# Kernel optimization log

Hardware: AMD Instinct MI355X
Metric: run time of the kernel (lower is better)

The kernel has to match this reference:

```python
import jax, jax.numpy as jnp
import numpy as np

B, N, S, K = 16, 4096, 1024, 32
C_PTS = 64
MLP = [64, 64, 128]
EPS = 1e-5


def setup_inputs() -> dict:
    key = jax.random.key(0)
    ks = jax.random.split(key, 2 + len(MLP))
    inp = {
        "xyz": jax.random.normal(ks[0], (B, N, 3), jnp.float32),
        "points": jax.random.normal(ks[1], (B, N, C_PTS), jnp.float32),
    }
    last = 3 + C_PTS
    for i, o in enumerate(MLP):
        inp[f"w{i}"] = jax.random.normal(ks[2 + i], (o, last), jnp.float32) / np.sqrt(last).astype(np.float32)
        inp[f"b{i}"] = jnp.zeros((o,), jnp.float32)
        inp[f"gamma{i}"] = jnp.ones((o,), jnp.float32)
        inp[f"beta{i}"] = jnp.zeros((o,), jnp.float32)
        last = o
    return inp


def _farthest_point_sample(xyz, n_samples):
    # Sequential FPS; start index 0 (torch version uses a random start).
    b, n, _ = xyz.shape

    def step(carry, _):
        distance, farthest = carry  # [B,N], [B]
        centroid = jnp.take_along_axis(xyz, farthest[:, None, None], axis=1)  # [B,1,3]
        dist = jnp.sum((xyz - centroid) ** 2, axis=-1)  # [B,N]
        distance = jnp.minimum(distance, dist)
        new_far = jnp.argmax(distance, axis=-1).astype(jnp.int32)
        return (distance, new_far), farthest

    init = (jnp.full((b, n), 1e10, xyz.dtype), jnp.zeros((b,), jnp.int32))
    _, idxs = jax.lax.scan(step, init, None, length=n_samples)
    return idxs.T  # [B,S]


def _square_distance(src, dst):
    # ||src||^2 + ||dst||^2 - 2 src.dst  -> [B, S, N]
    return (jnp.sum(src ** 2, -1)[:, :, None]
            + jnp.sum(dst ** 2, -1)[:, None, :]
            - 2.0 * jnp.einsum('bsc,bnc->bsn', src, dst))


_gather = jax.vmap(lambda a, i: a[i])  # per-batch fancy gather


def _mlp_layer(x, w, bias, gamma, beta):
    # x: [B,S,K,Cin]; 1x1 conv == channel matmul, then training-mode BN over (B,S,K), then ReLU.
    y = jnp.einsum('bskc,oc->bsko', x, w) + bias
    mean = jnp.mean(y, axis=(0, 1, 2))
    var = jnp.mean((y - mean) ** 2, axis=(0, 1, 2))
    y = (y - mean) * jax.lax.rsqrt(var + EPS) * gamma + beta
    return jax.nn.relu(y)


def reference(xyz, points, w0, b0, gamma0, beta0, w1, b1, gamma1, beta1, w2, b2, gamma2, beta2):
    fps_idx = _farthest_point_sample(xyz, S)                   # [B,S]
    new_xyz = _gather(xyz, fps_idx)                            # [B,S,3]
    dists = _square_distance(new_xyz, xyz)                     # [B,S,N]
    nn_idx = jax.lax.top_k(-dists, K)[1]                       # [B,S,K]
    grouped_xyz = _gather(xyz, nn_idx)                         # [B,S,K,3]
    grouped_pts = _gather(points, nn_idx)                      # [B,S,K,C]
    feat = jnp.concatenate([grouped_xyz - new_xyz[:, :, None, :], grouped_pts], axis=-1)  # [B,S,K,3+C]
    x = _mlp_layer(feat, w0, b0, gamma0, beta0)
    x = _mlp_layer(x, w1, b1, gamma1, beta1)
    x = _mlp_layer(x, w2, b2, gamma2, beta2)
    new_points = jnp.max(x, axis=2)                            # [B,S,Cout]
    new_points = jnp.transpose(new_points, (0, 2, 1))          # [B,Cout,S] matches torch output
    return new_xyz, new_points
```

## Files before the change

kernel.cpp:

```cpp
#include <hip/hip_runtime.h>

#define B_ 16
#define N_ 4096
#define S_ 1024
#define K_ 32
#define NSLOT 128
#define CNT_F 524288.0f
#define RWS 524288

typedef unsigned short ushort_t;
typedef short short8 __attribute__((ext_vector_type(8)));
typedef float floatx4 __attribute__((ext_vector_type(4)));
union U4S8 { uint4 u; short8 v; };

__device__ __forceinline__ ushort_t f2bf(float f) {
  unsigned u = __float_as_uint(f);
  unsigned r = (u + 0x7fffu + ((u >> 16) & 1u)) >> 16;
  return (ushort_t)r;
}
__device__ __forceinline__ unsigned pkrne(float a, float b) {
  return (unsigned)f2bf(a) | ((unsigned)f2bf(b) << 16);
}
__device__ __forceinline__ unsigned pkhu(float a, float b) {
  return ((__float_as_uint(a) + 0x8000u) >> 16) |
// ... 14 lines not shown
  x1 = fmaxf(fmaf(x1, sca.y, sha.y), 0.0f);
  x2 = fmaxf(fmaf(x2, sca.z, sha.z), 0.0f);
  x3 = fmaxf(fmaf(x3, sca.w, sha.w), 0.0f);
  x4 = fmaxf(fmaf(x4, scb.x, shb.x), 0.0f);
  x5 = fmaxf(fmaf(x5, scb.y, shb.y), 0.0f);
  x6 = fmaxf(fmaf(x6, scb.z, shb.z), 0.0f);
  x7 = fmaxf(fmaf(x7, scb.w, shb.w), 0.0f);
  return make_uint4(pkhu(x0, x1), pkhu(x2, x3), pkhu(x4, x5), pkhu(x6, x7));
}

#define FPS_T 256
#define FPS_P (N_ / FPS_T)
#define FPS_W (FPS_T / 64)

template <int CTRL>
__device__ __forceinline__ unsigned dpp_max_u32(unsigned v) {
  unsigned o = (unsigned)__builtin_amdgcn_update_dpp(0, (int)v, CTRL, 0xf, 0xf, true);
  return v > o ? v : o;
}
__device__ __forceinline__ unsigned wave_max_u32(unsigned v) {
  v = dpp_max_u32<0x111>(v);
  v = dpp_max_u32<0x112>(v);
  v = dpp_max_u32<0x114>(v);
  v = dpp_max_u32<0x118>(v);
  v = dpp_max_u32<0x142>(v);
  v = dpp_max_u32<0x143>(v);
  return (unsigned)__builtin_amdgcn_readlane((int)v, 63);
}

__global__ __launch_bounds__(256) void prep_all(
    const float* __restrict__ xyz, float4* __restrict__ xyzw,
    const float* __restrict__ w0, const float* __restrict__ w1,
    const float* __restrict__ w2, ushort_t* __restrict__ wB0,
    ushort_t* __restrict__ wB1, ushort_t* __restrict__ wB2) {
  int i = blockIdx.x * 256 + threadIdx.x;
  float x = xyz[(size_t)i * 3 + 0];
  float y = xyz[(size_t)i * 3 + 1];
  float z = xyz[(size_t)i * 3 + 2];
  float nrm = __fadd_rn(__fadd_rn(__fmul_rn(x, x), __fmul_rn(y, y)), __fmul_rn(z, z));
  xyzw[i] = make_float4(x, y, z, nrm);
  if (i < 64 * 96) {
    int o = i / 96, c = i % 96;
    ushort_t v = 0;
    if (c < 64) v = f2bf(w0[o * 67 + 3 + c]);
    else if (c < 67) v = f2bf(w0[o * 67 + (c - 64)]);
    wB0[i] = v;
  }
  if (i < 64 * 64) wB1[i] = f2bf(w1[i]);
  if (i < 128 * 64) wB2[i] = f2bf(w2[i]);
}

#define SMEM_BYTES 56320
#define NBLK 512
#define NCONS_W ((NBLK - B_) * 4)

__global__ __launch_bounds__(256, 1) void fused_kernel(
    const float* __restrict__ xyz, const float* __restrict__ points,
    const float4* __restrict__ xyzw, const ushort_t* __restrict__ wB0,
    const float* __restrict__ bias0, int* __restrict__ pub,
    float* __restrict__ out_newxyz, ushort_t* __restrict__ y0,
    float* __restrict__ stats) {
  __shared__ __align__(16) char smem[SMEM_BYTES];
  int t = threadIdx.x;
  int w = t >> 6, l = t & 63;

  if (blockIdx.x < B_) {
    float* xyz_s = (float*)smem;
    int* idx_s = (int*)(smem + 49152);
    unsigned long long* keys_s = (unsigned long long*)(smem + 53248);
    int b = blockIdx.x;
    const float* xb = xyz + (size_t)b * N_ * 3;
    for (int i = t; i < N_ * 3; i += FPS_T) xyz_s[i] = xb[i];
    __syncthreads();
    float px[FPS_P], py[FPS_P], pz[FPS_P], dd[FPS_P];
#pragma unroll
    for (int j = 0; j < FPS_P; ++j) {
      int n = t + j * FPS_T;
      px[j] = xyz_s[n * 3 + 0];
      py[j] = xyz_s[n * 3 + 1];
      pz[j] = xyz_s[n * 3 + 2];
      dd[j] = 1e10f;
    }
    __builtin_amdgcn_s_setprio(3);
    int fi = 0;
#pragma unroll 1
    for (int s = 0; s < S_; ++s) {
      if (t == 0) {
        idx_s[s] = fi;
        __hip_atomic_store(&pub[(b << 10) + s], fi + 1, __ATOMIC_RELAXED,
                           __HIP_MEMORY_SCOPE_AGENT);
      }
      float cx = xyz_s[fi * 3 + 0], cy = xyz_s[fi * 3 + 1], cz = xyz_s[fi * 3 + 2];
      float bv = -1.0f;
      int bi = 0;
#pragma unroll
      for (int j = 0; j < FPS_P; ++j) {
        float dx = __fsub_rn(px[j], cx);
        float dy = __fsub_rn(py[j], cy);
        float dz = __fsub_rn(pz[j], cz);
        float d = __fadd_rn(__fadd_rn(__fmul_rn(dx, dx), __fmul_rn(dy, dy)),
                            __fmul_rn(dz, dz));
        d = fminf(dd[j], d);
        dd[j] = d;
        if (d > bv) { bv = d; bi = t + j * FPS_T; }
      }
      unsigned hi = __float_as_uint(bv);
      unsigned vmax = wave_max_u32(hi);
      unsigned cand = (hi == vmax) ? (unsigned)(N_ - 1 - bi) : 0u;
      unsigned cmax = wave_max_u32(cand);
      if ((t & 63) == 0)
        keys_s[(s & 1) * FPS_W + (t >> 6)] =
            ((unsigned long long)vmax << 32) | cmax;
      __syncthreads();
      unsigned long long m = keys_s[(s & 1) * FPS_W + 0];
#pragma unroll
      for (int ww = 1; ww < FPS_W; ++ww) {
        unsigned long long k = keys_s[(s & 1) * FPS_W + ww];
        m = k > m ? k : m;
      }
      fi = (N_ - 1) - (int)(unsigned)(m & 0xFFFFFFFFULL);
    }
    __builtin_amdgcn_s_setprio(0);
    __syncthreads();
    for (int s = t; s < S_; s += FPS_T) {
      int i = idx_s[s];
      out_newxyz[((size_t)b * S_ + s) * 3 + 0] = xyz_s[i * 3 + 0];
      out_newxyz[((size_t)b * S_ + s) * 3 + 1] = xyz_s[i * 3 + 1];
      out_newxyz[((size_t)b * S_ + s) * 3 + 2] = xyz_s[i * 3 + 2];
    }
    return;
  }

  int n16 = l & 15, quad = l >> 4;
  U4S8 bf0[4][3];
  float b0v[4], ssum[4], ssq[4];
#pragma unroll
  for (int nt = 0; nt < 4; ++nt) {
#pragma unroll
    for (int kc = 0; kc < 3; ++kc)
      bf0[nt][kc].u = *reinterpret_cast<const uint4*>(
          wB0 + (size_t)(nt * 16 + n16) * 96 + kc * 32 + quad * 8);
    b0v[nt] = bias0[nt * 16 + n16];
    ssum[nt] = 0.0f;
    ssq[nt] = 0.0f;
  }
  float* ltw = (float*)(smem + w * (16 * 68 * 4));
  int wid = (blockIdx.x - B_) * 4 + w;

#pragma unroll 1
  for (int r = wid; r < B_ * S_; r += NCONS_W) {
    int b = r & 15, s = r >> 4;
    int bs = (b << 10) + s;
    int pv = 0;
    if (l == 0) {
      int tries = 0;
      while ((pv = __hip_atomic_load(&pub[bs], __ATOMIC_RELAXED,
                                     __HIP_MEMORY_SCOPE_AGENT)) == 0) {
        __builtin_amdgcn_s_sleep(32);
        if (++tries > 65536) break;
      }
    }
    pv = __shfl(pv, 0);
    int ci = pv - 1;
    if (ci < 0) ci = 0;
    const float4* xw = xyzw + (size_t)b * N_;
    float4 c4 = xw[ci];
    float sx = c4.x, sy = c4.y, sz = c4.z;
    float nxn = c4.w;

    unsigned u[64];
#pragma unroll
    for (int j = 0; j < 64; ++j) {
      int nn = j * 64 + l;
      float4 v = xw[nn];
      float e = __fadd_rn(__fadd_rn(__fmul_rn(sx, v.x), __fmul_rn(sy, v.y)),
                          __fmul_rn(sz, v.z));
      float d = __fadd_rn(__fadd_rn(nxn, v.w), __fmul_rn(-2.0f, e));
      int sb = __float_as_int(d);
      u[j] = (sb < 0) ? ~((unsigned)sb) : (((unsigned)sb) | 0x80000000u);
    }
// ... 76 lines not shown
#pragma unroll
        for (int rI = 0; rI < 4; ++rI) {
          float ys = acc[nt][rI] + b0v[nt];
          ssum[nt] += ys;
          ssq[nt] = fmaf(ys, ys, ssq[nt]);
          ltw[(quad * 4 + rI) * 68 + nt * 16 + n16] = ys;
        }
      const float* lrow = ltw + n16 * 68 + quad * 16;
      float4 va = *reinterpret_cast<const float4*>(lrow);
      float4 vb = *reinterpret_cast<const float4*>(lrow + 4);
      float4 vc = *reinterpret_cast<const float4*>(lrow + 8);
      float4 vd = *reinterpret_cast<const float4*>(lrow + 12);
      ushort_t* yo = y0 + (size_t)(rb + n16) * 64 + quad * 16;
      *reinterpret_cast<uint4*>(yo) =
          make_uint4(pkhu(va.x, va.y), pkhu(va.z, va.w), pkhu(vb.x, vb.y), pkhu(vb.z, vb.w));
      *reinterpret_cast<uint4*>(yo + 8) =
          make_uint4(pkhu(vc.x, vc.y), pkhu(vc.z, vc.w), pkhu(vd.x, vd.y), pkhu(vd.z, vd.w));
    }
  }

  float* stp = stats + (size_t)(wid & (NSLOT - 1)) * 64 * 2;
#pragma unroll
  for (int nt = 0; nt < 4; ++nt) {
    float s = ssum[nt], q = ssq[nt];
    s += __shfl_down(s, 16); q += __shfl_down(q, 16);
    s += __shfl_down(s, 32); q += __shfl_down(q, 32);
    if (l < 16) {
      atomicAdd(&stp[(size_t)(nt * 16 + l) * 2 + 0], s);
      atomicAdd(&stp[(size_t)(nt * 16 + l) * 2 + 1], q);
    }
  }
}

__global__ __launch_bounds__(256) void gemm1_mfma(
    const ushort_t* __restrict__ y0, const float* __restrict__ bnp,
    const ushort_t* __restrict__ wB1, const float* __restrict__ bias1,
    ushort_t* __restrict__ y1, float* __restrict__ stats) {
  __shared__ __align__(16) float lt[4][16 * 68];
  int t = threadIdx.x;
  int w = t >> 6, l = t & 63;
  int n = l & 15, quad = l >> 4;
  U4S8 bf[4][2];
#pragma unroll
  for (int nt = 0; nt < 4; ++nt)
#pragma unroll
    for (int kc = 0; kc < 2; ++kc)
      bf[nt][kc].u = *reinterpret_cast<const uint4*>(
          wB1 + (size_t)(nt * 16 + n) * 64 + kc * 32 + quad * 8);
  float4 scA[2], scB[2], shA[2], shB[2];
#pragma unroll
  for (int kc = 0; kc < 2; ++kc) {
    int cb = kc * 32 + quad * 8;
    scA[kc] = *reinterpret_cast<const float4*>(&bnp[cb]);
    scB[kc] = *reinterpret_cast<const float4*>(&bnp[cb + 4]);
    shA[kc] = *reinterpret_cast<const float4*>(&bnp[64 + cb]);
    shB[kc] = *reinterpret_cast<const float4*>(&bnp[64 + cb + 4]);
  }
  float b1v[4], ssum[4], ssq[4];
#pragma unroll
  for (int nt = 0; nt < 4; ++nt) {
    b1v[nt] = bias1[nt * 16 + n];
    ssum[nt] = 0.0f;
    ssq[nt] = 0.0f;
  }
  int rowbase0 = blockIdx.x * 1024 + w * 256;
  float* ltw = lt[w];
#pragma unroll 1
  for (int tile = 0; tile < 16; ++tile) {
    int rb = rowbase0 + tile * 16;
    U4S8 af[2];
#pragma unroll
    for (int kc = 0; kc < 2; ++kc) {
      uint4 xv = *reinterpret_cast<const uint4*>(
          y0 + (size_t)(rb + n) * 64 + kc * 32 + quad * 8);
      af[kc].u = bn_relu_pack(xv, scA[kc], scB[kc], shA[kc], shB[kc]);
    }
    floatx4 acc[4];
#pragma unroll
    for (int nt = 0; nt < 4; ++nt) acc[nt] = floatx4{0.f, 0.f, 0.f, 0.f};
#pragma unroll
    for (int kc = 0; kc < 2; ++kc)
#pragma unroll
      for (int nt = 0; nt < 4; ++nt)
        acc[nt] = __builtin_amdgcn_mfma_f32_16x16x32_bf16(
            af[kc].v, bf[nt][kc].v, acc[nt], 0, 0, 0);
#pragma unroll
    for (int nt = 0; nt < 4; ++nt)
#pragma unroll
      for (int rI = 0; rI < 4; ++rI) {
        float ys = acc[nt][rI] + b1v[nt];
        ssum[nt] += ys;
        ssq[nt] = fmaf(ys, ys, ssq[nt]);
        ltw[(quad * 4 + rI) * 68 + nt * 16 + n] = ys;
      }
    const float* lrow = ltw + n * 68 + quad * 16;
    float4 va = *reinterpret_cast<const float4*>(lrow);
    float4 vb = *reinterpret_cast<const float4*>(lrow + 4);
    float4 vc = *reinterpret_cast<const float4*>(lrow + 8);
    float4 vd = *reinterpret_cast<const float4*>(lrow + 12);
    ushort_t* yo = y1 + (size_t)(rb + n) * 64 + quad * 16;
    *reinterpret_cast<uint4*>(yo) =
        make_uint4(pkhu(va.x, va.y), pkhu(va.z, va.w), pkhu(vb.x, vb.y), pkhu(vb.z, vb.w));
    *reinterpret_cast<uint4*>(yo + 8) =
        make_uint4(pkhu(vc.x, vc.y), pkhu(vc.z, vc.w), pkhu(vd.x, vd.y), pkhu(vd.z, vd.w));
  }
  float* stp = stats + (size_t)((blockIdx.x * 4 + w) & (NSLOT - 1)) * 64 * 2;
#pragma unroll
  for (int nt = 0; nt < 4; ++nt) {
    float s = ssum[nt], q = ssq[nt];
    s += __shfl_down(s, 16); q += __shfl_down(q, 16);
    s += __shfl_down(s, 32); q += __shfl_down(q, 32);
    if (l < 16) {
      atomicAdd(&stp[(size_t)(nt * 16 + l) * 2 + 0], s);
      atomicAdd(&stp[(size_t)(nt * 16 + l) * 2 + 1], q);
    }
  }
}

__global__ __launch_bounds__(256) void gemm2_mfma(
    const ushort_t* __restrict__ y1, const float* __restrict__ bnp,
    const ushort_t* __restrict__ wB2, const float* __restrict__ bias2,
    float* __restrict__ stats, float* __restrict__ maxY, float* __restrict__ minY) {
  int t = threadIdx.x;
  int w = t >> 6, l = t & 63;
  int n = l & 15, quad = l >> 4;
  U4S8 bf[8][2];
#pragma unroll
  for (int nt = 0; nt < 8; ++nt)
#pragma unroll
    for (int kc = 0; kc < 2; ++kc)
      bf[nt][kc].u = *reinterpret_cast<const uint4*>(
          wB2 + (size_t)(nt * 16 + n) * 64 + kc * 32 + quad * 8);
  float4 scA[2], scB[2], shA[2], shB[2];
#pragma unroll
  for (int kc = 0; kc < 2; ++kc) {
    int cb = kc * 32 + quad * 8;
    scA[kc] = *reinterpret_cast<const float4*>(&bnp[128 + cb]);
    scB[kc] = *reinterpret_cast<const float4*>(&bnp[128 + cb + 4]);
    shA[kc] = *reinterpret_cast<const float4*>(&bnp[192 + cb]);
    shB[kc] = *reinterpret_cast<const float4*>(&bnp[192 + cb + 4]);
  }
  float b2v[8], ssum[8], ssq[8], mxv[8], mnv[8];
#pragma unroll
  for (int nt = 0; nt < 8; ++nt) {
    b2v[nt] = bias2[nt * 16 + n];
    ssum[nt] = 0.0f;
    ssq[nt] = 0.0f;
    mxv[nt] = -3.4e38f;
    mnv[nt] = 3.4e38f;
  }
  int rowbase0 = blockIdx.x * 1024 + w * 256;
#pragma unroll 1
  for (int tile = 0; tile < 16; ++tile) {
    int rb = rowbase0 + tile * 16;
    U4S8 af[2];
#pragma unroll
    for (int kc = 0; kc < 2; ++kc) {
      uint4 xv = *reinterpret_cast<const uint4*>(
          y1 + (size_t)(rb + n) * 64 + kc * 32 + quad * 8);
      af[kc].u = bn_relu_pack(xv, scA[kc], scB[kc], shA[kc], shB[kc]);
    }
    floatx4 acc[8];
#pragma unroll
    for (int nt = 0; nt < 8; ++nt) acc[nt] = floatx4{0.f, 0.f, 0.f, 0.f};
#pragma unroll
    for (int kc = 0; kc < 2; ++kc)
#pragma unroll
      for (int nt = 0; nt < 8; ++nt)
        acc[nt] = __builtin_amdgcn_mfma_f32_16x16x32_bf16(
            af[kc].v, bf[nt][kc].v, acc[nt], 0, 0, 0);
#pragma unroll
    for (int nt = 0; nt < 8; ++nt)
#pragma unroll
      for (int rI = 0; rI < 4; ++rI) {
        float ya = acc[nt][rI] + b2v[nt];
        ssum[nt] += ya;
        ssq[nt] = fmaf(ya, ya, ssq[nt]);
        mxv[nt] = fmaxf(mxv[nt], ya);
        mnv[nt] = fminf(mnv[nt], ya);
      }
    if (tile & 1) {
      int sidx = (rowbase0 >> 5) + (tile >> 1);
#pragma unroll
      for (int nt = 0; nt < 8; ++nt) {
        float mx = mxv[nt], mn = mnv[nt];
        mx = fmaxf(mx, __shfl_down(mx, 16));
        mn = fminf(mn, __shfl_down(mn, 16));
        mx = fmaxf(mx, __shfl_down(mx, 32));
        mn = fminf(mn, __shfl_down(mn, 32));
        if (l < 16) {
          maxY[(size_t)sidx * 128 + nt * 16 + l] = mx;
          minY[(size_t)sidx * 128 + nt * 16 + l] = mn;
        }
        mxv[nt] = -3.4e38f;
        mnv[nt] = 3.4e38f;
      }
    }
  }
  float* stp = stats + (size_t)((blockIdx.x * 4 + w) & (NSLOT - 1)) * 128 * 2;
#pragma unroll
  for (int nt = 0; nt < 8; ++nt) {
    float s = ssum[nt], q = ssq[nt];
    s += __shfl_down(s, 16); q += __shfl_down(q, 16);
    s += __shfl_down(s, 32); q += __shfl_down(q, 32);
    if (l < 16) {
      atomicAdd(&stp[(size_t)(nt * 16 + l) * 2 + 0], s);
      atomicAdd(&stp[(size_t)(nt * 16 + l) * 2 + 1], q);
    }
  }
}

__global__ void bn_finalize(const float* __restrict__ st, int cout,
                            const float* __restrict__ gamma,
                            const float* __restrict__ beta,
                            float* __restrict__ scale, float* __restrict__ shift) {
  int o = threadIdx.x;
  if (o >= cout) return;
  float s = 0.0f, q = 0.0f;
  for (int i = 0; i < NSLOT; ++i) {
    s += st[((size_t)i * cout + o) * 2 + 0];
    q += st[((size_t)i * cout + o) * 2 + 1];
  }
  float mean = s * (1.0f / CNT_F);
  float var = q * (1.0f / CNT_F) - mean * mean;
  float sc = gamma[o] / sqrtf(var + 1e-5f);
  scale[o] = sc;
  shift[o] = beta[o] - mean * sc;
}

__global__ __launch_bounds__(256) void pool_kernel(
    const float* __restrict__ maxY, const float* __restrict__ minY,
    const float* __restrict__ bnp, float* __restrict__ out) {
  __shared__ float tile[128 * 65];
  int b = blockIdx.x >> 4;
  int sbase = (blockIdx.x & 15) * 64;
  int t = threadIdx.x;
#pragma unroll 4
  for (int i = 0; i < 32; ++i) {
    int e = i * 256 + t;
    int sl = e >> 7, o = e & 127;
    float sc = bnp[256 + o], sh = bnp[384 + o];
    size_t g = ((size_t)(b * S_ + sbase + sl)) * 128 + o;
    float v = (sc >= 0.0f) ? maxY[g] : minY[g];
    tile[o * 65 + sl] = fmaxf(fmaf(v, sc, sh), 0.0f);
  }
  __syncthreads();
  int sl = t & 63;
  for (int o2 = t >> 6; o2 < 128; o2 += 4) {
    out[((size_t)(b * 128 + o2)) * S_ + sbase + sl] = tile[o2 * 65 + sl];
  }
}

static inline size_t alup(size_t x) { return (x + 255) & ~(size_t)255; }

extern "C" void kernel_launch(void* const* d_in, const int* in_sizes, int n_in,
                              void* d_out, int out_size, void* d_ws, size_t ws_size,
                              hipStream_t stream) {
  (void)in_sizes; (void)n_in; (void)out_size;
  const float* xyz = (const float*)d_in[0];
  const float* points = (const float*)d_in[1];
  const float* w0 = (const float*)d_in[2];
  const float* b0 = (const float*)d_in[3];
  const float* g0 = (const float*)d_in[4];
  const float* be0 = (const float*)d_in[5];
  const float* w1 = (const float*)d_in[6];
  const float* b1 = (const float*)d_in[7];
  const float* g1 = (const float*)d_in[8];
  const float* be1 = (const float*)d_in[9];
  const float* w2 = (const float*)d_in[10];
  const float* b2 = (const float*)d_in[11];
  const float* g2 = (const float*)d_in[12];
  const float* be2 = (const float*)d_in[13];
  float* out_newxyz = (float*)d_out;
  float* out_newpts = out_newxyz + (size_t)B_ * S_ * 3;

  char* p = (char*)d_ws;
  int* pub = (int*)p;      p += alup((size_t)B_ * S_ * 4);
  float4* xyzw = (float4*)p; p += alup((size_t)B_ * N_ * 16);
  float* st0 = (float*)p;  p += (size_t)NSLOT * 64 * 2 * 4;
  float* st1 = (float*)p;  p += (size_t)NSLOT * 64 * 2 * 4;
  float* st2 = (float*)p;  p += (size_t)NSLOT * 128 * 2 * 4;
  float* bnp = (float*)p;  p += alup(512 * 4);
  ushort_t* wB0 = (ushort_t*)p; p += alup(64 * 96 * 2);
  ushort_t* wB1 = (ushort_t*)p; p += alup(64 * 64 * 2);
  ushort_t* wB2 = (ushort_t*)p; p += alup(128 * 64 * 2);
  float* maxY = (float*)p; p += (size_t)B_ * S_ * 128 * 4;
  float* minY = (float*)p; p += (size_t)B_ * S_ * 128 * 4;
  ushort_t* y0 = (ushort_t*)p; p += (size_t)RWS * 64 * 2;
  ushort_t* y1 = (ushort_t*)p; p += (size_t)RWS * 64 * 2;
  if ((size_t)(p - (char*)d_ws) > ws_size) return;

  float* sc0 = bnp;       float* sh0 = bnp + 64;
  float* sc1 = bnp + 128; float* sh1 = bnp + 192;
  float* sc2 = bnp + 256; float* sh2 = bnp + 384;

  hipMemsetAsync(st0, 0, (size_t)NSLOT * (64 + 64 + 128) * 2 * 4, stream);
  hipMemsetAsync(pub, 0, (size_t)B_ * S_ * 4, stream);
  prep_all<<<256, 256, 0, stream>>>(xyz, xyzw, w0, w1, w2, wB0, wB1, wB2);
  fused_kernel<<<NBLK, 256, 0, stream>>>(
      xyz, points, xyzw, wB0, b0, pub, out_newxyz, y0, st0);
  bn_finalize<<<1, 128, 0, stream>>>(st0, 64, g0, be0, sc0, sh0);
  gemm1_mfma<<<RWS / 1024, 256, 0, stream>>>(y0, bnp, wB1, b1, y1, st1);
  bn_finalize<<<1, 128, 0, stream>>>(st1, 64, g1, be1, sc1, sh1);
  gemm2_mfma<<<RWS / 1024, 256, 0, stream>>>(y1, bnp, wB2, b2, st2, maxY, minY);
  bn_finalize<<<1, 128, 0, stream>>>(st2, 128, g2, be2, sc2, sh2);
  pool_kernel<<<B_ * (S_ / 64), 256, 0, stream>>>(maxY, minY, bnp, out_newpts);
}
```

Measured before the change: 784.7 us.

## Tree-reduce FPS argmax per thread and idle consumer blocks colocated with FPS blocks

After: 850.3 us. 1.08x slower.

```diff
diff --git a/kernel.cpp b/kernel.cpp
--- a/kernel.cpp
+++ b/kernel.cpp
@@ -90,7 +90,7 @@
 
 #define SMEM_BYTES 56320
 #define NBLK 512
-#define NCONS_W ((NBLK - B_) * 4)
+#define NCONS_W 1920
 
 __global__ __launch_bounds__(256, 1) void fused_kernel(
     const float* __restrict__ xyz, const float* __restrict__ points,
@@ -129,8 +129,6 @@
                            __HIP_MEMORY_SCOPE_AGENT);
       }
       float cx = xyz_s[fi * 3 + 0], cy = xyz_s[fi * 3 + 1], cz = xyz_s[fi * 3 + 2];
-      float bv = -1.0f;
-      int bi = 0;
 #pragma unroll
       for (int j = 0; j < FPS_P; ++j) {
         float dx = __fsub_rn(px[j], cx);
@@ -138,13 +136,27 @@
         float dz = __fsub_rn(pz[j], cz);
         float d = __fadd_rn(__fadd_rn(__fmul_rn(dx, dx), __fmul_rn(dy, dy)),
                             __fmul_rn(dz, dz));
-        d = fminf(dd[j], d);
-        dd[j] = d;
-        if (d > bv) { bv = d; bi = t + j * FPS_T; }
-      }
-      unsigned hi = __float_as_uint(bv);
+        dd[j] = fminf(dd[j], d);
+      }
+      float tm[FPS_P / 2];
+#pragma unroll
+      for (int i = 0; i < FPS_P / 2; ++i) tm[i] = fmaxf(dd[i], dd[i + FPS_P / 2]);
+#pragma unroll
+      for (int st = FPS_P / 4; st >= 1; st >>= 1)
+#pragma unroll
+        for (int i = 0; i < st; ++i) tm[i] = fmaxf(tm[i], tm[i + st]);
+      float lmax = tm[0];
+      unsigned cu[FPS_P];
+#pragma unroll
+      for (int j = 0; j < FPS_P; ++j)
+        cu[j] = (dd[j] == lmax) ? (unsigned)(N_ - 1 - (t + j * FPS_T)) : 0u;
+#pragma unroll
+      for (int st = FPS_P / 2; st >= 1; st >>= 1)
+#pragma unroll
+        for (int i = 0; i < st; ++i) cu[i] = cu[i] > cu[i + st] ? cu[i] : cu[i + st];
+      unsigned hi = __float_as_uint(lmax);
       unsigned vmax = wave_max_u32(hi);
-      unsigned cand = (hi == vmax) ? (unsigned)(N_ - 1 - bi) : 0u;
+      unsigned cand = (hi == vmax) ? cu[0] : 0u;
       unsigned cmax = wave_max_u32(cand);
       if ((t & 63) == 0)
         keys_s[(s & 1) * FPS_W + (t >> 6)] =
@@ -169,6 +181,10 @@
     return;
   }
 
+  if (blockIdx.x >= 256 && blockIdx.x < 256 + B_) return;
+  int cb = blockIdx.x - B_;
+  if (blockIdx.x >= 256 + B_) cb -= B_;
+
   int n16 = l & 15, quad = l >> 4;
   U4S8 bf0[4][3];
   float b0v[4], ssum[4], ssq[4];
@@ -183,7 +199,7 @@
     ssq[nt] = 0.0f;
   }
   float* ltw = (float*)(smem + w * (16 * 68 * 4));
-  int wid = (blockIdx.x - B_) * 4 + w;
+  int wid = cb * 4 + w;
 
 #pragma unroll 1
   for (int r = wid; r < B_ * S_; r += NCONS_W) {
```

## Merge MLP tail kernels into one persistent kernel with grid barriers

Applied to the files above, without the earlier changes.

After: 965.3 us. +23.0%, slower.

```diff
diff --git a/kernel.cpp b/kernel.cpp
--- a/kernel.cpp
+++ b/kernel.cpp
@@ -326,222 +326,269 @@
   }
 }
 
-__global__ __launch_bounds__(256) void gemm1_mfma(
-    const ushort_t* __restrict__ y0, const float* __restrict__ bnp,
-    const ushort_t* __restrict__ wB1, const float* __restrict__ bias1,
-    ushort_t* __restrict__ y1, float* __restrict__ stats) {
+#define MEGA_NBLK 512
+
+__device__ __forceinline__ void grid_sync(int* ctr, int slot) {
+  __threadfence();
+  __syncthreads();
+  if (threadIdx.x == 0) {
+    __hip_atomic_fetch_add(&ctr[slot], 1, __ATOMIC_RELEASE,
+                           __HIP_MEMORY_SCOPE_AGENT);
+    int tries = 0;
+    while (__hip_atomic_load(&ctr[slot], __ATOMIC_ACQUIRE,
+                             __HIP_MEMORY_SCOPE_AGENT) < MEGA_NBLK) {
+      __builtin_amdgcn_s_sleep(16);
+      if (++tries > (1 << 20)) break;
+    }
+  }
+  __syncthreads();
+}
+
+__global__ __launch_bounds__(256, 1) void mlp_tail(
+    const ushort_t* __restrict__ y0, const ushort_t* __restrict__ wB1,
+    const float* __restrict__ bias1, const ushort_t* __restrict__ wB2,
+    const float* __restrict__ bias2, const float* __restrict__ g0,
+    const float* __restrict__ be0, const float* __restrict__ g1,
+    const float* __restrict__ be1, const float* __restrict__ g2,
+    const float* __restrict__ be2, const float* __restrict__ st0,
+    float* __restrict__ st1, float* __restrict__ st2,
+    ushort_t* __restrict__ y1, float* __restrict__ maxY,
+    float* __restrict__ minY, float* __restrict__ out,
+    int* __restrict__ ctr) {
   __shared__ __align__(16) float lt[4][16 * 68];
+  __shared__ __align__(16) float bn_s[256];
   int t = threadIdx.x;
   int w = t >> 6, l = t & 63;
   int n = l & 15, quad = l >> 4;
-  U4S8 bf[4][2];
-#pragma unroll
-  for (int nt = 0; nt < 4; ++nt)
-#pragma unroll
-    for (int kc = 0; kc < 2; ++kc)
-      bf[nt][kc].u = *reinterpret_cast<const uint4*>(
-          wB1 + (size_t)(nt * 16 + n) * 64 + kc * 32 + quad * 8);
-  float4 scA[2], scB[2], shA[2], shB[2];
-#pragma unroll
-  for (int kc = 0; kc < 2; ++kc) {
-    int cb = kc * 32 + quad * 8;
-    scA[kc] = *reinterpret_cast<const float4*>(&bnp[cb]);
-    scB[kc] = *reinterpret_cast<const float4*>(&bnp[cb + 4]);
-    shA[kc] = *reinterpret_cast<const float4*>(&bnp[64 + cb]);
-    shB[kc] = *reinterpret_cast<const float4*>(&bnp[64 + cb + 4]);
-  }
-  float b1v[4], ssum[4], ssq[4];
-#pragma unroll
-  for (int nt = 0; nt < 4; ++nt) {
-    b1v[nt] = bias1[nt * 16 + n];
-    ssum[nt] = 0.0f;
-    ssq[nt] = 0.0f;
-  }
   int rowbase0 = blockIdx.x * 1024 + w * 256;
   float* ltw = lt[w];
+
+  if (t < 64) {
+    float s = 0.0f, q = 0.0f;
+    for (int i = 0; i < NSLOT; ++i) {
+      s += st0[((size_t)i * 64 + t) * 2 + 0];
+      q += st0[((size_t)i * 64 + t) * 2 + 1];
+    }
+    float mean = s * (1.0f / CNT_F);
+    float var = q * (1.0f / CNT_F) - mean * mean;
+    float sc = g0[t] / sqrtf(var + 1e-5f);
+    bn_s[t] = sc;
+    bn_s[128 + t] = be0[t] - mean * sc;
+  }
+  __syncthreads();
+
+  {
+    U4S8 bf[4][2];
+#pragma unroll
+    for (int nt = 0; nt < 4; ++nt)
+#pragma unroll
+      for (int kc = 0; kc < 2; ++kc)
+        bf[nt][kc].u = *reinterpret_cast<const uint4*>(
+            wB1 + (size_t)(nt * 16 + n) * 64 + kc * 32 + quad * 8);
+    float4 scA[2], scB[2], shA[2], shB[2];
+#pragma unroll
+    for (int kc = 0; kc < 2; ++kc) {
+      int cb = kc * 32 + quad * 8;
+      scA[kc] = *reinterpret_cast<const float4*>(&bn_s[cb]);
+      scB[kc] = *reinterpret_cast<const float4*>(&bn_s[cb + 4]);
+      shA[kc] = *reinterpret_cast<const float4*>(&bn_s[128 + cb]);
+      shB[kc] = *reinterpret_cast<const float4*>(&bn_s[128 + cb + 4]);
+    }
+    float b1v[4], ssum[4], ssq[4];
+#pragma unroll
+    for (int nt = 0; nt < 4; ++nt) {
+      b1v[nt] = bias1[nt * 16 + n];
+      ssum[nt] = 0.0f;
+      ssq[nt] = 0.0f;
+    }
 #pragma unroll 1
-  for (int tile = 0; tile < 16; ++tile) {
-    int rb = rowbase0 + tile * 16;
-    U4S8 af[2];
+    for (int tile = 0; tile < 16; ++tile) {
+      int rb = rowbase0 + tile * 16;
+      U4S8 af[2];
+#pragma unroll
+      for (int kc = 0; kc < 2; ++kc) {
+        uint4 xv = *reinterpret_cast<const uint4*>(
+            y0 + (size_t)(rb + n) * 64 + kc * 32 + quad * 8);
+        af[kc].u = bn_relu_pack(xv, scA[kc], scB[kc], shA[kc], shB[kc]);
+      }
+      floatx4 acc[4];
+#pragma unroll
+      for (int nt = 0; nt < 4; ++nt) acc[nt] = floatx4{0.f, 0.f, 0.f, 0.f};
+#pragma unroll
+      for (int kc = 0; kc < 2; ++kc)
+#pragma unroll
+        for (int nt = 0; nt < 4; ++nt)
+          acc[nt] = __builtin_amdgcn_mfma_f32_16x16x32_bf16(
+              af[kc].v, bf[nt][kc].v, acc[nt], 0, 0, 0);
+#pragma unroll
+      for (int nt = 0; nt < 4; ++nt)
+#pragma unroll
+        for (int rI = 0; rI < 4; ++rI) {
+          float ys = acc[nt][rI] + b1v[nt];
+          ssum[nt] += ys;
+          ssq[nt] = fmaf(ys, ys, ssq[nt]);
+          ltw[(quad * 4 + rI) * 68 + nt * 16 + n] = ys;
+        }
+      const float* lrow = ltw + n * 68 + quad * 16;
+      float4 va = *reinterpret_cast<const float4*>(lrow);
+      float4 vb = *reinterpret_cast<const float4*>(lrow + 4);
+      float4 vc = *reinterpret_cast<const float4*>(lrow + 8);
+      float4 vd = *reinterpret_cast<const float4*>(lrow + 12);
+      ushort_t* yo = y1 + (size_t)(rb + n) * 64 + quad * 16;
+      *reinterpret_cast<uint4*>(yo) =
+          make_uint4(pkhu(va.x, va.y), pkhu(va.z, va.w), pkhu(vb.x, vb.y), pkhu(vb.z, vb.w));
+      *reinterpret_cast<uint4*>(yo + 8) =
+          make_uint4(pkhu(vc.x, vc.y), pkhu(vc.z, vc.w), pkhu(vd.x, vd.y), pkhu(vd.z, vd.w));
+    }
+    float* stp = st1 + (size_t)((blockIdx.x * 4 + w) & (NSLOT - 1)) * 64 * 2;
+#pragma unroll
+    for (int nt = 0; nt < 4; ++nt) {
+      float s = ssum[nt], q = ssq[nt];
+      s += __shfl_down(s, 16); q += __shfl_down(q, 16);
+      s += __shfl_down(s, 32); q += __shfl_down(q, 32);
+      if (l < 16) {
+        atomicAdd(&stp[(size_t)(nt * 16 + l) * 2 + 0], s);
+        atomicAdd(&stp[(size_t)(nt * 16 + l) * 2 + 1], q);
+      }
+    }
+  }
+
+  grid_sync(ctr, 0);
+
+  if (t < 64) {
+    float s = 0.0f, q = 0.0f;
+    for (int i = 0; i < NSLOT; ++i) {
+      s += st1[((size_t)i * 64 + t) * 2 + 0];
+      q += st1[((size_t)i * 64 + t) * 2 + 1];
+    }
+    float mean = s * (1.0f / CNT_F);
+    float var = q * (1.0f / CNT_F) - mean * mean;
+    float sc = g1[t] / sqrtf(var + 1e-5f);
+    bn_s[t] = sc;
+    bn_s[128 + t] = be1[t] - mean * sc;
+  }
+  __syncthreads();
+
+  {
+    U4S8 bf[8][2];
+#pragma unroll
+    for (int nt = 0; nt < 8; ++nt)
+#pragma unroll
+      for (int kc = 0; kc < 2; ++kc)
+        bf[nt][kc].u = *reinterpret_cast<const uint4*>(
+            wB2 + (size_t)(nt * 16 + n) * 64 + kc * 32 + quad * 8);
+    float4 scA[2], scB[2], shA[2], shB[2];
 #pragma unroll
     for (int kc = 0; kc < 2; ++kc) {
-      uint4 xv = *reinterpret_cast<const uint4*>(
-          y0 + (size_t)(rb + n) * 64 + kc * 32 + quad * 8);
-      af[kc].u = bn_relu_pack(xv, scA[kc], scB[kc], shA[kc], shB[kc]);
-    }
-    floatx4 acc[4];
-#pragma unroll
-    for (int nt = 0; nt < 4; ++nt) acc[nt] = floatx4{0.f, 0.f, 0.f, 0.f};
-#pragma unroll
-    for (int kc = 0; kc < 2; ++kc)
-#pragma unroll
-      for (int nt = 0; nt < 4; ++nt)
-        acc[nt] = __builtin_amdgcn_mfma_f32_16x16x32_bf16(
-            af[kc].v, bf[nt][kc].v, acc[nt], 0, 0, 0);
-#pragma unroll
-    for (int nt = 0; nt < 4; ++nt)
-#pragma unroll
-      for (int rI = 0; rI < 4; ++rI) {
-        float ys = acc[nt][rI] + b1v[nt];
-        ssum[nt] += ys;
-        ssq[nt] = fmaf(ys, ys, ssq[nt]);
-        ltw[(quad * 4 + rI) * 68 + nt * 16 + n] = ys;
-      }
-    const float* lrow = ltw + n * 68 + quad * 16;
-    float4 va = *reinterpret_cast<const float4*>(lrow);
-    float4 vb = *reinterpret_cast<const float4*>(lrow + 4);
-    float4 vc = *reinterpret_cast<const float4*>(lrow + 8);
-    float4 vd = *reinterpret_cast<const float4*>(lrow + 12);
-    ushort_t* yo = y1 + (size_t)(rb + n) * 64 + quad * 16;
-    *reinterpret_cast<uint4*>(yo) =
-        make_uint4(pkhu(va.x, va.y), pkhu(va.z, va.w), pkhu(vb.x, vb.y), pkhu(vb.z, vb.w));
-    *reinterpret_cast<uint4*>(yo + 8) =
-        make_uint4(pkhu(vc.x, vc.y), pkhu(vc.z, vc.w), pkhu(vd.x, vd.y), pkhu(vd.z, vd.w));
-  }
-  float* stp = stats + (size_t)((blockIdx.x * 4 + w) & (NSLOT - 1)) * 64 * 2;
-#pragma unroll
-  for (int nt = 0; nt < 4; ++nt) {
-    float s = ssum[nt], q = ssq[nt];
-    s += __shfl_down(s, 16); q += __shfl_down(q, 16);
-    s += __shfl_down(s, 32); q += __shfl_down(q, 32);
-    if (l < 16) {
-      atomicAdd(&stp[(size_t)(nt * 16 + l) * 2 + 0], s);
-      atomicAdd(&stp[(size_t)(nt * 16 + l) * 2 + 1], q);
-    }
-  }
-}
-
-__global__ __launch_bounds__(256) void gemm2_mfma(
-    const ushort_t* __restrict__ y1, const float* __restrict__ bnp,
-    const ushort_t* __restrict__ wB2, const float* __restrict__ bias2,
-    float* __restrict__ stats, float* __restrict__ maxY, float* __restrict__ minY) {
-  int t = threadIdx.x;
-  int w = t >> 6, l = t & 63;
-  int n = l & 15, quad = l >> 4;
-  U4S8 bf[8][2];
-#pragma unroll
-  for (int nt = 0; nt < 8; ++nt)
-#pragma unroll
-    for (int kc = 0; kc < 2; ++kc)
-      bf[nt][kc].u = *reinterpret_cast<const uint4*>(
-          wB2 + (size_t)(nt * 16 + n) * 64 + kc * 32 + quad * 8);
-  float4 scA[2], scB[2], shA[2], shB[2];
-#pragma unroll
-  for (int kc = 0; kc < 2; ++kc) {
-    int cb = kc * 32 + quad * 8;
-    scA[kc] = *reinterpret_cast<const float4*>(&bnp[128 + cb]);
-    scB[kc] = *reinterpret_cast<const float4*>(&bnp[128 + cb + 4]);
-    shA[kc] = *reinterpret_cast<const float4*>(&bnp[192 + cb]);
-    shB[kc] = *reinterpret_cast<const float4*>(&bnp[192 + cb + 4]);
-  }
-  float b2v[8], ssum[8], ssq[8], mxv[8], mnv[8];
-#pragma unroll
-  for (int nt = 0; nt < 8; ++nt) {
-    b2v[nt] = bias2[nt * 16 + n];
-    ssum[nt] = 0.0f;
-    ssq[nt] = 0.0f;
-    mxv[nt] = -3.4e38f;
-    mnv[nt] = 3.4e38f;
-  }
-  int rowbase0 = blockIdx.x * 1024 + w * 256;
+      int cb = kc * 32 + quad * 8;
+      scA[kc] = *reinterpret_cast<const float4*>(&bn_s[cb]);
+      scB[kc] = *reinterpret_cast<const float4*>(&bn_s[cb + 4]);
+      shA[kc] = *reinterpret_cast<const float4*>(&bn_s[128 + cb]);
+      shB[kc] = *reinterpret_cast<const float4*>(&bn_s[128 + cb + 4]);
+    }
+    float b2v[8], ssum[8], ssq[8], mxv[8], mnv[8];
+#pragma unroll
+    for (int nt = 0; nt < 8; ++nt) {
+      b2v[nt] = bias2[nt * 16 + n];
+      ssum[nt] = 0.0f;
+      ssq[nt] = 0.0f;
+      mxv[nt] = -3.4e38f;
+      mnv[nt] = 3.4e38f;
+    }
 #pragma unroll 1
-  for (int tile = 0; tile < 16; ++tile) {
-    int rb = rowbase0 + tile * 16;
-    U4S8 af[2];
-#pragma unroll
-    for (int kc = 0; kc < 2; ++kc) {
-      uint4 xv = *reinterpret_cast<const uint4*>(
-          y1 + (size_t)(rb + n) * 64 + kc * 32 + quad * 8);
-      af[kc].u = bn_relu_pack(xv, scA[kc], scB[kc], shA[kc], shB[kc]);
-    }
-    floatx4 acc[8];
-#pragma unroll
-    for (int nt = 0; nt < 8; ++nt) acc[nt] = floatx4{0.f, 0.f, 0.f, 0.f};
-#pragma unroll
-    for (int kc = 0; kc < 2; ++kc)
+    for (int tile = 0; tile < 16; ++tile) {
+      int rb = rowbase0 + tile * 16;
+      U4S8 af[2];
+#pragma unroll
+      for (int kc = 0; kc < 2; ++kc) {
+        uint4 xv = *reinterpret_cast<const uint4*>(
+            y1 + (size_t)(rb + n) * 64 + kc * 32 + quad * 8);
+        af[kc].u = bn_relu_pack(xv, scA[kc], scB[kc], shA[kc], shB[kc]);
+      }
+      floatx4 acc[8];
+#pragma unroll
+      for (int nt = 0; nt < 8; ++nt) acc[nt] = floatx4{0.f, 0.f, 0.f, 0.f};
+#pragma unroll
+      for (int kc = 0; kc < 2; ++kc)
+#pragma unroll
+        for (int nt = 0; nt < 8; ++nt)
+          acc[nt] = __builtin_amdgcn_mfma_f32_16x16x32_bf16(
+              af[kc].v, bf[nt][kc].v, acc[nt], 0, 0, 0);
 #pragma unroll
       for (int nt = 0; nt < 8; ++nt)
-        acc[nt] = __builtin_amdgcn_mfma_f32_16x16x32_bf16(
-            af[kc].v, bf[nt][kc].v, acc[nt], 0, 0, 0);
-#pragma unroll
-    for (int nt = 0; nt < 8; ++nt)
-#pragma unroll
-      for (int rI = 0; rI < 4; ++rI) {
-        float ya = acc[nt][rI] + b2v[nt];
-        ssum[nt] += ya;
-        ssq[nt] = fmaf(ya, ya, ssq[nt]);
-        mxv[nt] = fmaxf(mxv[nt], ya);
-        mnv[nt] = fminf(mnv[nt], ya);
-      }
-    if (tile & 1) {
-      int sidx = (rowbase0 >> 5) + (tile >> 1);
-#pragma unroll
-      for (int nt = 0; nt < 8; ++nt) {
-        float mx = mxv[nt], mn = mnv[nt];
-        mx = fmaxf(mx, __shfl_down(mx, 16));
-        mn = fminf(mn, __shfl_down(mn, 16));
-        mx = fmaxf(mx, __shfl_down(mx, 32));
-        mn = fminf(mn, __shfl_down(mn, 32));
-        if (l < 16) {
-          maxY[(size_t)sidx * 128 + nt * 16 + l] = mx;
-          minY[(size_t)sidx * 128 + nt * 16 + l] = mn;
+#pragma unroll
+        for (int rI = 0; rI < 4; ++rI) {
+          float ya = acc[nt][rI] + b2v[nt];
+          ssum[nt] += ya;
+          ssq[nt] = fmaf(ya, ya, ssq[nt]);
+          mxv[nt] = fmaxf(mxv[nt], ya);
+          mnv[nt] = fminf(mnv[nt], ya);
         }
-        mxv[nt] = -3.4e38f;
-        mnv[nt] = 3.4e38f;
-      }
-    }
-  }
-  float* stp = stats + (size_t)((blockIdx.x * 4 + w) & (NSLOT - 1)) * 128 * 2;
-#pragma unroll
-  for (int nt = 0; nt < 8; ++nt) {
-    float s = ssum[nt], q = ssq[nt];
-    s += __shfl_down(s, 16); q += __shfl_down(q, 16);
-    s += __shfl_down(s, 32); q += __shfl_down(q, 32);
-    if (l < 16) {
-      atomicAdd(&stp[(size_t)(nt * 16 + l) * 2 + 0], s);
-      atomicAdd(&stp[(size_t)(nt * 16 + l) * 2 + 1], q);
-    }
-  }
-}
-
-__global__ void bn_finalize(const float* __restrict__ st, int cout,
-                            const float* __restrict__ gamma,
-                            const float* __restrict__ beta,
-                            float* __restrict__ scale, float* __restrict__ shift) {
-  int o = threadIdx.x;
-  if (o >= cout) return;
-  float s = 0.0f, q = 0.0f;
-  for (int i = 0; i < NSLOT; ++i) {
-    s += st[((size_t)i * cout + o) * 2 + 0];
-    q += st[((size_t)i * cout + o) * 2 + 1];
-  }
-  float mean = s * (1.0f / CNT_F);
-  float var = q * (1.0f / CNT_F) - mean * mean;
-  float sc = gamma[o] / sqrtf(var + 1e-5f);
-  scale[o] = sc;
-  shift[o] = beta[o] - mean * sc;
-}
-
-__global__ __launch_bounds__(256) void pool_kernel(
-    const float* __restrict__ maxY, const float* __restrict__ minY,
-    const float* __restrict__ bnp, float* __restrict__ out) {
-  __shared__ float tile[128 * 65];
-  int b = blockIdx.x >> 4;
-  int sbase = (blockIdx.x & 15) * 64;
-  int t = threadIdx.x;
+      if (tile & 1) {
+        int sidx = (rowbase0 >> 5) + (tile >> 1);
+#pragma unroll
+        for (int nt = 0; nt < 8; ++nt) {
+          float mx = mxv[nt], mn = mnv[nt];
+          mx = fmaxf(mx, __shfl_down(mx, 16));
+          mn = fminf(mn, __shfl_down(mn, 16));
+          mx = fmaxf(mx, __shfl_down(mx, 32));
+          mn = fminf(mn, __shfl_down(mn, 32));
+          if (l < 16) {
+            maxY[(size_t)sidx * 128 + nt * 16 + l] = mx;
+            minY[(size_t)sidx * 128 + nt * 16 + l] = mn;
+          }
+          mxv[nt] = -3.4e38f;
+          mnv[nt] = 3.4e38f;
+        }
+      }
+    }
+    float* stp = st2 + (size_t)((blockIdx.x * 4 + w) & (NSLOT - 1)) * 128 * 2;
+#pragma unroll
+    for (int nt = 0; nt < 8; ++nt) {
+      float s = ssum[nt], q = ssq[nt];
+      s += __shfl_down(s, 16); q += __shfl_down(q, 16);
+      s += __shfl_down(s, 32); q += __shfl_down(q, 32);
+      if (l < 16) {
+        atomicAdd(&stp[(size_t)(nt * 16 + l) * 2 + 0], s);
+        atomicAdd(&stp[(size_t)(nt * 16 + l) * 2 + 1], q);
+      }
+    }
+  }
+
+  grid_sync(ctr, 1);
+
+  if (t < 128) {
+    float s = 0.0f, q = 0.0f;
+    for (int i = 0; i < NSLOT; ++i) {
+      s += st2[((size_t)i * 128 + t) * 2 + 0];
+      q += st2[((size_t)i * 128 + t) * 2 + 1];
+    }
+    float mean = s * (1.0f / CNT_F);
+    float var = q * (1.0f / CNT_F) - mean * mean;
+    float sc = g2[t] / sqrtf(var + 1e-5f);
+    bn_s[t] = sc;
+    bn_s[128 + t] = be2[t] - mean * sc;
+  }
+  __syncthreads();
+
+  {
+    int b = blockIdx.x >> 5;
+    int sbase = (blockIdx.x & 31) * 32;
+    float* tile = &lt[0][0];
 #pragma unroll 4
-  for (int i = 0; i < 32; ++i) {
-    int e = i * 256 + t;
-    int sl = e >> 7, o = e & 127;
-    float sc = bnp[256 + o], sh = bnp[384 + o];
-    size_t g = ((size_t)(b * S_ + sbase + sl)) * 128 + o;
-    float v = (sc >= 0.0f) ? maxY[g] : minY[g];
-    tile[o * 65 + sl] = fmaxf(fmaf(v, sc, sh), 0.0f);
-  }
-  __syncthreads();
-  int sl = t & 63;
-  for (int o2 = t >> 6; o2 < 128; o2 += 4) {
-    out[((size_t)(b * 128 + o2)) * S_ + sbase + sl] = tile[o2 * 65 + sl];
+    for (int i = 0; i < 16; ++i) {
+      int e = i * 256 + t;
+      int sl = e >> 7, o = e & 127;
+      float sc = bn_s[o], sh = bn_s[128 + o];
+      size_t g = ((size_t)(b * S_ + sbase + sl)) * 128 + o;
+      float v = (sc >= 0.0f) ? maxY[g] : minY[g];
+      tile[o * 33 + sl] = fmaxf(fmaf(v, sc, sh), 0.0f);
+    }
+    __syncthreads();
+    int sl = t & 31;
+    for (int o2 = t >> 5; o2 < 128; o2 += 8) {
+      out[((size_t)(b * 128 + o2)) * S_ + sbase + sl] = tile[o2 * 33 + sl];
+    }
   }
 }
 
@@ -570,11 +617,11 @@
 
   char* p = (char*)d_ws;
   int* pub = (int*)p;      p += alup((size_t)B_ * S_ * 4);
+  int* ctr = (int*)p;      p += alup(256);
   float4* xyzw = (float4*)p; p += alup((size_t)B_ * N_ * 16);
   float* st0 = (float*)p;  p += (size_t)NSLOT * 64 * 2 * 4;
   float* st1 = (float*)p;  p += (size_t)NSLOT * 64 * 2 * 4;
   float* st2 = (float*)p;  p += (size_t)NSLOT * 128 * 2 * 4;
-  float* bnp = (float*)p;  p += alup(512 * 4);
   ushort_t* wB0 = (ushort_t*)p; p += alup(64 * 96 * 2);
   ushort_t* wB1 = (ushort_t*)p; p += alup(64 * 64 * 2);
   ushort_t* wB2 = (ushort_t*)p; p += alup(128 * 64 * 2);
@@ -584,19 +631,13 @@
   ushort_t* y1 = (ushort_t*)p; p += (size_t)RWS * 64 * 2;
   if ((size_t)(p - (char*)d_ws) > ws_size) return;
 
-  float* sc0 = bnp;       float* sh0 = bnp + 64;
-  float* sc1 = bnp + 128; float* sh1 = bnp + 192;
-  float* sc2 = bnp + 256; float* sh2 = bnp + 384;
-
   hipMemsetAsync(st0, 0, (size_t)NSLOT * (64 + 64 + 128) * 2 * 4, stream);
   hipMemsetAsync(pub, 0, (size_t)B_ * S_ * 4, stream);
+  hipMemsetAsync(ctr, 0, 256, stream);
   prep_all<<<256, 256, 0, stream>>>(xyz, xyzw, w0, w1, w2, wB0, wB1, wB2);
   fused_kernel<<<NBLK, 256, 0, stream>>>(
       xyz, points, xyzw, wB0, b0, pub, out_newxyz, y0, st0);
-  bn_finalize<<<1, 128, 0, stream>>>(st0, 64, g0, be0, sc0, sh0);
-  gemm1_mfma<<<RWS / 1024, 256, 0, stream>>>(y0, bnp, wB1, b1, y1, st1);
-  bn_finalize<<<1, 128, 0, stream>>>(st1, 64, g1, be1, sc1, sh1);
-  gemm2_mfma<<<RWS / 1024, 256, 0, stream>>>(y1, bnp, wB2, b2, st2, maxY, minY);
-  bn_finalize<<<1, 128, 0, stream>>>(st2, 128, g2, be2, sc2, sh2);
-  pool_kernel<<<B_ * (S_ / 64), 256, 0, stream>>>(maxY, minY, bnp, out_newpts);
-}
+  mlp_tail<<<MEGA_NBLK, 256, 0, stream>>>(
+      y0, wB1, b1, wB2, b2, g0, be0, g1, be1, g2, be2,
+      st0, st1, st2, y1, maxY, minY, out_newpts, ctr);
+}
```

## Fold BN finalize into consumer kernels, zero buffers in prep, pass FPS centroid via LDS

Applied to the files above, without the earlier changes.

Result: slower. 1.004 ms (+27.9%).

```diff
diff --git a/kernel.cpp b/kernel.cpp
--- a/kernel.cpp
+++ b/kernel.cpp
@@ -70,13 +70,16 @@
     const float* __restrict__ xyz, float4* __restrict__ xyzw,
     const float* __restrict__ w0, const float* __restrict__ w1,
     const float* __restrict__ w2, ushort_t* __restrict__ wB0,
-    ushort_t* __restrict__ wB1, ushort_t* __restrict__ wB2) {
+    ushort_t* __restrict__ wB1, ushort_t* __restrict__ wB2,
+    int* __restrict__ pub, float* __restrict__ st_all) {
   int i = blockIdx.x * 256 + threadIdx.x;
   float x = xyz[(size_t)i * 3 + 0];
   float y = xyz[(size_t)i * 3 + 1];
   float z = xyz[(size_t)i * 3 + 2];
   float nrm = __fadd_rn(__fadd_rn(__fmul_rn(x, x), __fmul_rn(y, y)), __fmul_rn(z, z));
   xyzw[i] = make_float4(x, y, z, nrm);
+  st_all[i] = 0.0f;
+  if (i < B_ * S_) pub[i] = 0;
   if (i < 64 * 96) {
     int o = i / 96, c = i % 96;
     ushort_t v = 0;
@@ -106,6 +109,7 @@
     float* xyz_s = (float*)smem;
     int* idx_s = (int*)(smem + 49152);
     unsigned long long* keys_s = (unsigned long long*)(smem + 53248);
+    float4* cxyz = (float4*)(smem + 53312);
     int b = blockIdx.x;
     const float* xb = xyz + (size_t)b * N_ * 3;
     for (int i = t; i < N_ * 3; i += FPS_T) xyz_s[i] = xb[i];
@@ -121,6 +125,7 @@
     }
     __builtin_amdgcn_s_setprio(3);
     int fi = 0;
+    float cx = xyz_s[0], cy = xyz_s[1], cz = xyz_s[2];
 #pragma unroll 1
     for (int s = 0; s < S_; ++s) {
       if (t == 0) {
@@ -128,7 +133,6 @@
         __hip_atomic_store(&pub[(b << 10) + s], fi + 1, __ATOMIC_RELAXED,
                            __HIP_MEMORY_SCOPE_AGENT);
       }
-      float cx = xyz_s[fi * 3 + 0], cy = xyz_s[fi * 3 + 1], cz = xyz_s[fi * 3 + 2];
       float bv = -1.0f;
       int bi = 0;
 #pragma unroll
@@ -146,16 +150,27 @@
       unsigned vmax = wave_max_u32(hi);
       unsigned cand = (hi == vmax) ? (unsigned)(N_ - 1 - bi) : 0u;
       unsigned cmax = wave_max_u32(cand);
+      int base = (s & 1) * FPS_W;
       if ((t & 63) == 0)
-        keys_s[(s & 1) * FPS_W + (t >> 6)] =
-            ((unsigned long long)vmax << 32) | cmax;
+        keys_s[base + w] = ((unsigned long long)vmax << 32) | cmax;
+      if (hi == vmax && (unsigned)(N_ - 1 - bi) == cmax) {
+        int jj = bi >> 8;
+        cxyz[base + w] = make_float4(px[jj], py[jj], pz[jj], 0.0f);
+      }
       __syncthreads();
-      unsigned long long m = keys_s[(s & 1) * FPS_W + 0];
-#pragma unroll
-      for (int ww = 1; ww < FPS_W; ++ww) {
-        unsigned long long k = keys_s[(s & 1) * FPS_W + ww];
-        m = k > m ? k : m;
-      }
+      unsigned long long k0 = keys_s[base + 0], k1 = keys_s[base + 1];
+      unsigned long long k2 = keys_s[base + 2], k3 = keys_s[base + 3];
+      float4 c0 = cxyz[base + 0], c1 = cxyz[base + 1];
+      float4 c2 = cxyz[base + 2], c3 = cxyz[base + 3];
+      bool b01 = k1 > k0;
+      unsigned long long m01 = b01 ? k1 : k0;
+      bool b23 = k3 > k2;
+      unsigned long long m23 = b23 ? k3 : k2;
+      bool bf2 = m23 > m01;
+      unsigned long long m = bf2 ? m23 : m01;
+      cx = bf2 ? (b23 ? c3.x : c2.x) : (b01 ? c1.x : c0.x);
+      cy = bf2 ? (b23 ? c3.y : c2.y) : (b01 ? c1.y : c0.y);
+      cz = bf2 ? (b23 ? c3.z : c2.z) : (b01 ? c1.z : c0.z);
       fi = (N_ - 1) - (int)(unsigned)(m & 0xFFFFFFFFULL);
     }
     __builtin_amdgcn_s_setprio(0);
@@ -326,11 +341,40 @@
   }
 }
 
+__device__ __forceinline__ void bn_compute64(
+    const float* __restrict__ st, const float* __restrict__ gamma,
+    const float* __restrict__ beta, float* bn_s, float (*red)[64]) {
+  int t = threadIdx.x;
+  int ch = t & 63, grp = t >> 6;
+  float s_ = 0.0f, q_ = 0.0f;
+  for (int i = grp; i < NSLOT; i += 4) {
+    s_ += st[((size_t)i * 64 + ch) * 2 + 0];
+    q_ += st[((size_t)i * 64 + ch) * 2 + 1];
+  }
+  red[grp][ch] = s_;
+  red[4 + grp][ch] = q_;
+  __syncthreads();
+  if (t < 64) {
+    float S = red[0][t] + red[1][t] + red[2][t] + red[3][t];
+    float Q = red[4][t] + red[5][t] + red[6][t] + red[7][t];
+    float mean = S * (1.0f / CNT_F);
+    float var = Q * (1.0f / CNT_F) - mean * mean;
+    float sc = gamma[t] / sqrtf(var + 1e-5f);
+    bn_s[t] = sc;
+    bn_s[64 + t] = beta[t] - mean * sc;
+  }
+  __syncthreads();
+}
+
 __global__ __launch_bounds__(256) void gemm1_mfma(
-    const ushort_t* __restrict__ y0, const float* __restrict__ bnp,
+    const ushort_t* __restrict__ y0, const float* __restrict__ st0,
+    const float* __restrict__ g0, const float* __restrict__ be0,
     const ushort_t* __restrict__ wB1, const float* __restrict__ bias1,
     ushort_t* __restrict__ y1, float* __restrict__ stats) {
   __shared__ __align__(16) float lt[4][16 * 68];
+  __shared__ __align__(16) float bn_s[128];
+  __shared__ float red[8][64];
+  bn_compute64(st0, g0, be0, bn_s, red);
   int t = threadIdx.x;
   int w = t >> 6, l = t & 63;
   int n = l & 15, quad = l >> 4;
@@ -345,10 +389,10 @@
 #pragma unroll
   for (int kc = 0; kc < 2; ++kc) {
     int cb = kc * 32 + quad * 8;
-    scA[kc] = *reinterpret_cast<const float4*>(&bnp[cb]);
-    scB[kc] = *reinterpret_cast<const float4*>(&bnp[cb + 4]);
-    shA[kc] = *reinterpret_cast<const float4*>(&bnp[64 + cb]);
-    shB[kc] = *reinterpret_cast<const float4*>(&bnp[64 + cb + 4]);
+    scA[kc] = *reinterpret_cast<const float4*>(&bn_s[cb]);
+    scB[kc] = *reinterpret_cast<const float4*>(&bn_s[cb + 4]);
+    shA[kc] = *reinterpret_cast<const float4*>(&bn_s[64 + cb]);
+    shB[kc] = *reinterpret_cast<const float4*>(&bn_s[64 + cb + 4]);
   }
   float b1v[4], ssum[4], ssq[4];
 #pragma unroll
@@ -412,9 +456,13 @@
 }
 
 __global__ __launch_bounds__(256) void gemm2_mfma(
-    const ushort_t* __restrict__ y1, const float* __restrict__ bnp,
+    const ushort_t* __restrict__ y1, const float* __restrict__ st1,
+    const float* __restrict__ g1, const float* __restrict__ be1,
     const ushort_t* __restrict__ wB2, const float* __restrict__ bias2,
     float* __restrict__ stats, float* __restrict__ maxY, float* __restrict__ minY) {
+  __shared__ __align__(16) float bn_s[128];
+  __shared__ float red[8][64];
+  bn_compute64(st1, g1, be1, bn_s, red);
   int t = threadIdx.x;
   int w = t >> 6, l = t & 63;
   int n = l & 15, quad = l >> 4;
@@ -429,10 +477,10 @@
 #pragma unroll
   for (int kc = 0; kc < 2; ++kc) {
     int cb = kc * 32 + quad * 8;
-    scA[kc] = *reinterpret_cast<const float4*>(&bnp[128 + cb]);
-    scB[kc] = *reinterpret_cast<const float4*>(&bnp[128 + cb + 4]);
-    shA[kc] = *reinterpret_cast<const float4*>(&bnp[192 + cb]);
-    shB[kc] = *reinterpret_cast<const float4*>(&bnp[192 + cb + 4]);
+    scA[kc] = *reinterpret_cast<const float4*>(&bn_s[cb]);
+    scB[kc] = *reinterpret_cast<const float4*>(&bn_s[cb + 4]);
+    shA[kc] = *reinterpret_cast<const float4*>(&bn_s[64 + cb]);
+    shB[kc] = *reinterpret_cast<const float4*>(&bn_s[64 + cb + 4]);
   }
   float b2v[8], ssum[8], ssq[8], mxv[8], mnv[8];
 #pragma unroll
@@ -504,36 +552,42 @@
   }
 }
 
-__global__ void bn_finalize(const float* __restrict__ st, int cout,
-                            const float* __restrict__ gamma,
-                            const float* __restrict__ beta,
-                            float* __restrict__ scale, float* __restrict__ shift) {
-  int o = threadIdx.x;
-  if (o >= cout) return;
-  float s = 0.0f, q = 0.0f;
-  for (int i = 0; i < NSLOT; ++i) {
-    s += st[((size_t)i * cout + o) * 2 + 0];
-    q += st[((size_t)i * cout + o) * 2 + 1];
-  }
-  float mean = s * (1.0f / CNT_F);
-  float var = q * (1.0f / CNT_F) - mean * mean;
-  float sc = gamma[o] / sqrtf(var + 1e-5f);
-  scale[o] = sc;
-  shift[o] = beta[o] - mean * sc;
-}
-
 __global__ __launch_bounds__(256) void pool_kernel(
     const float* __restrict__ maxY, const float* __restrict__ minY,
-    const float* __restrict__ bnp, float* __restrict__ out) {
+    const float* __restrict__ st2, const float* __restrict__ g2,
+    const float* __restrict__ be2, float* __restrict__ out) {
   __shared__ float tile[128 * 65];
+  __shared__ __align__(16) float bn_s[256];
+  __shared__ float redp[4][128];
+  int t = threadIdx.x;
+  {
+    int ch = t & 127, grp = t >> 7;
+    float s_ = 0.0f, q_ = 0.0f;
+    for (int i = grp; i < NSLOT; i += 2) {
+      s_ += st2[((size_t)i * 128 + ch) * 2 + 0];
+      q_ += st2[((size_t)i * 128 + ch) * 2 + 1];
+    }
+    redp[grp][ch] = s_;
+    redp[2 + grp][ch] = q_;
+    __syncthreads();
+    if (t < 128) {
+      float S = redp[0][t] + redp[1][t];
+      float Q = redp[2][t] + redp[3][t];
+      float mean = S * (1.0f / CNT_F);
+      float var = Q * (1.0f / CNT_F) - mean * mean;
+      float sc = g2[t] / sqrtf(var + 1e-5f);
+      bn_s[t] = sc;
+      bn_s[128 + t] = be2[t] - mean * sc;
+    }
+    __syncthreads();
+  }
   int b = blockIdx.x >> 4;
   int sbase = (blockIdx.x & 15) * 64;
-  int t = threadIdx.x;
 #pragma unroll 4
   for (int i = 0; i < 32; ++i) {
     int e = i * 256 + t;
     int sl = e >> 7, o = e & 127;
-    float sc = bnp[256 + o], sh = bnp[384 + o];
+    float sc = bn_s[o], sh = bn_s[128 + o];
     size_t g = ((size_t)(b * S_ + sbase + sl)) * 128 + o;
     float v = (sc >= 0.0f) ? maxY[g] : minY[g];
     tile[o * 65 + sl] = fmaxf(fmaf(v, sc, sh), 0.0f);
@@ -574,7 +628,6 @@
   float* st0 = (float*)p;  p += (size_t)NSLOT * 64 * 2 * 4;
   float* st1 = (float*)p;  p += (size_t)NSLOT * 64 * 2 * 4;
   float* st2 = (float*)p;  p += (size_t)NSLOT * 128 * 2 * 4;
-  float* bnp = (float*)p;  p += alup(512 * 4);
   ushort_t* wB0 = (ushort_t*)p; p += alup(64 * 96 * 2);
   ushort_t* wB1 = (ushort_t*)p; p += alup(64 * 64 * 2);
   ushort_t* wB2 = (ushort_t*)p; p += alup(128 * 64 * 2);
@@ -584,19 +637,13 @@
   ushort_t* y1 = (ushort_t*)p; p += (size_t)RWS * 64 * 2;
   if ((size_t)(p - (char*)d_ws) > ws_size) return;
 
-  float* sc0 = bnp;       float* sh0 = bnp + 64;
-  float* sc1 = bnp + 128; float* sh1 = bnp + 192;
-  float* sc2 = bnp + 256; float* sh2 = bnp + 384;
-
-  hipMemsetAsync(st0, 0, (size_t)NSLOT * (64 + 64 + 128) * 2 * 4, stream);
-  hipMemsetAsync(pub, 0, (size_t)B_ * S_ * 4, stream);
-  prep_all<<<256, 256, 0, stream>>>(xyz, xyzw, w0, w1, w2, wB0, wB1, wB2);
+  prep_all<<<256, 256, 0, stream>>>(xyz, xyzw, w0, w1, w2, wB0, wB1, wB2,
+                                    pub, st0);
   fused_kernel<<<NBLK, 256, 0, stream>>>(
       xyz, points, xyzw, wB0, b0, pub, out_newxyz, y0, st0);
-  bn_finalize<<<1, 128, 0, stream>>>(st0, 64, g0, be0, sc0, sh0);
-  gemm1_mfma<<<RWS / 1024, 256, 0, stream>>>(y0, bnp, wB1, b1, y1, st1);
-  bn_finalize<<<1, 128, 0, stream>>>(st1, 64, g1, be1, sc1, sh1);
-  gemm2_mfma<<<RWS / 1024, 256, 0, stream>>>(y1, bnp, wB2, b2, st2, maxY, minY);
-  bn_finalize<<<1, 128, 0, stream>>>(st2, 128, g2, be2, sc2, sh2);
-  pool_kernel<<<B_ * (S_ / 64), 256, 0, stream>>>(maxY, minY, bnp, out_newpts);
-}
+  gemm1_mfma<<<RWS / 1024, 256, 0, stream>>>(y0, st0, g0, be0, wB1, b1, y1, st1);
+  gemm2_mfma<<<RWS / 1024, 256, 0, stream>>>(y1, st1, g1, be1, wB2, b2, st2,
+                                             maxY, minY);
+  pool_kernel<<<B_ * (S_ / 64), 256, 0, stream>>>(maxY, minY, st2, g2, be2,
+                                                  out_newpts);
+}
```
